# Kernel tuning notes

Measured on AMD Instinct MI355X. Metric: run time of the kernel, lower is better.

## Reference

```python
import jax, jax.numpy as jnp
import numpy as np

N_NODES = 20000
N_EDGES = 100000   # undirected input edges; make_directed doubles them
FEAT = 128
N_RBF = 20
NUM_CONV = 3
CUTOFF = 20.0
BOX = 10.0


def setup_inputs() -> dict:
    key = jax.random.key(0)
    ks = jax.random.split(key, 6)
    cg_xyz = jax.random.uniform(ks[0], (N_NODES, 3), jnp.float32) * BOX
    # random edges with no self-loops (avoid d=0 singularity in rbf/unit)
    src = jax.random.randint(ks[1], (N_EDGES,), 0, N_NODES)
    off = jax.random.randint(ks[2], (N_EDGES,), 1, N_NODES)
    CG_nbr_list = jnp.stack([src, (src + off) % N_NODES], axis=1)
    cg_s = jax.random.normal(ks[3], (N_NODES, FEAT), jnp.float32)

    def w(k, shape, fan_in):
        return (jax.random.normal(k, shape, jnp.float32) / np.float32(np.sqrt(fan_in)))
    kk = jax.random.split(ks[4], 7)
    params = dict(
        msg_W1=w(kk[0], (NUM_CONV, FEAT, FEAT), FEAT),
        msg_b1=jnp.zeros((NUM_CONV, FEAT), jnp.float32),
        msg_W2=w(kk[1], (NUM_CONV, 3 * FEAT, FEAT), FEAT),
        msg_b2=jnp.zeros((NUM_CONV, 3 * FEAT), jnp.float32),
        dist_W=w(kk[2], (NUM_CONV, 3 * FEAT, N_RBF), N_RBF),
        dist_b=jnp.zeros((NUM_CONV, 3 * FEAT), jnp.float32),
        upd_U=w(kk[3], (NUM_CONV, FEAT, FEAT), FEAT),
        upd_V=w(kk[4], (NUM_CONV, FEAT, FEAT), FEAT),
        upd_sW1=w(kk[5], (NUM_CONV, FEAT, 2 * FEAT), 2 * FEAT),
        upd_sb1=jnp.zeros((NUM_CONV, FEAT), jnp.float32),
        upd_sW2=w(kk[6], (NUM_CONV, 3 * FEAT, FEAT), FEAT),
        upd_sb2=jnp.zeros((NUM_CONV, 3 * FEAT), jnp.float32),
    )
    return dict(cg_xyz=cg_xyz, CG_nbr_list=CG_nbr_list, cg_s=cg_s, **params)


def _forward(cg_xyz, cg_s, nbr, msg_W1, msg_b1, msg_W2, msg_b2, dist_W, dist_b,
             upd_U, upd_V, upd_sW1, upd_sb1, upd_sW2, upd_sb2):
    N = cg_s.shape[0]
    # make_directed: input is undirected -> append flipped edges
    nbrs = jnp.concatenate([nbr, nbr[:, ::-1]], axis=0)   # [E, 2]
    i, j = nbrs[:, 0], nbrs[:, 1]
    r_ij = cg_xyz[j] - cg_xyz[i]                           # [E, 3]
    d = jnp.linalg.norm(r_ij, axis=-1)                     # [E]
    unit = r_ij / d[:, None]
    # PainnRadialBasis: sin(k*pi*d/cutoff)/d, k=1..n_rbf
    kvec = jnp.arange(1, N_RBF + 1, dtype=cg_xyz.dtype)
    rbf = jnp.sin(kvec * jnp.pi * d[:, None] / CUTOFF) / d[:, None]   # [E, n_rbf]
    # cosine envelope
    env = jnp.where(d < CUTOFF, 0.5 * (jnp.cos(jnp.pi * d / CUTOFF) + 1.0), 0.0)

    s = cg_s
    v = jnp.zeros((N, FEAT, 3), cg_s.dtype)
    for l in range(NUM_CONV):
        # ---- MessageBlock ----
        phi = jax.nn.silu(s @ msg_W1[l].T + msg_b1[l]) @ msg_W2[l].T + msg_b2[l]  # [N, 3F]
        w_s = (rbf @ dist_W[l].T + dist_b[l]) * env[:, None]                      # [E, 3F]
        inv = (phi[j] * w_s).reshape(-1, 3, FEAT)                                 # [E, 3, F]
        dv_ij = inv[:, 2, :, None] * unit[:, None, :] + inv[:, 0, :, None] * v[j] # [E, F, 3]
        s = s + jax.ops.segment_sum(inv[:, 1, :], i, num_segments=N)
        v = v + jax.ops.segment_sum(dv_ij, i, num_segments=N)
        # ---- UpdateBlock ----
        u_v = jnp.einsum('nfd,gf->ngd', v, upd_U[l])   # [N, F, 3]
        v_v = jnp.einsum('nfd,gf->ngd', v, upd_V[l])
        v_v_norm = jnp.linalg.norm(v_v, axis=-1)       # [N, F]
        a = (jax.nn.silu(jnp.concatenate([s, v_v_norm], -1) @ upd_sW1[l].T + upd_sb1[l])
             @ upd_sW2[l].T + upd_sb2[l]).reshape(-1, 3, FEAT)  # a_vv, a_sv, a_ss
        s = s + (u_v * v_v).sum(-1) * a[:, 1, :] + a[:, 2, :]
        v = v + u_v * a[:, 0, :, None]
    return s, v


def reference(cg_xyz, CG_nbr_list, cg_s, msg_W1, msg_b1, msg_W2, msg_b2, dist_W,
              dist_b, upd_U, upd_V, upd_sW1, upd_sb1, upd_sW2, upd_sb2):
    return _forward(cg_xyz, cg_s, CG_nbr_list, msg_W1, msg_b1, msg_W2, msg_b2,
                    dist_W, dist_b, upd_U, upd_V, upd_sW1, upd_sb1, upd_sW2, upd_sb2)
```

## Files before the change

### kernel.cpp

```cpp
#include <hip/hip_runtime.h>
#include <math.h>

#define FEAT 128
#define NRBF 20
#define NCONV 3
#define PI_F 3.14159265358979323846f

typedef __attribute__((ext_vector_type(8))) short short8;
typedef __attribute__((ext_vector_type(4))) float floatx4;
typedef unsigned short ushort_t;

__device__ inline float b2f(unsigned short u) {
    union { unsigned int i; float f; } c; c.i = ((unsigned int)u) << 16; return c.f;
}
__device__ inline unsigned short f2b(float x) {
    union { float f; unsigned int i; } c; c.f = x;
    unsigned int u = c.i;
    return (unsigned short)((u + 0x7fffu + ((u >> 16) & 1u)) >> 16);
}

template<int MODE>
__global__ __launch_bounds__(256, 2) void mlp_fused_kernel(
    const float* __restrict__ s, const float* __restrict__ vv,
    const ushort_t* __restrict__ W1h, const ushort_t* __restrict__ W1l,
    const float* __restrict__ b1,
    const ushort_t* __restrict__ W2h, const ushort_t* __restrict__ W2l,
    const float* __restrict__ b2,
    ushort_t* __restrict__ out_b,
    const float* __restrict__ uv,
    float* s_out, float* vbuf,
    float* outv,
    const ushort_t* __restrict__ pW1h, const ushort_t* __restrict__ pW1l,
    const float* __restrict__ pb1,
    const ushort_t* __restrict__ pW2h, const ushort_t* __restrict__ pW2l,
    const float* __restrict__ pb2,
    ushort_t* __restrict__ pout,
    int M, int K1, int SP)
{
    __shared__ __align__(16) ushort_t Ah[64 * 40];
    __shared__ __align__(16) ushort_t Al[64 * 40];
    __shared__ __align__(16) ushort_t Wh[128 * 40];
    __shared__ __align__(16) ushort_t Wl[128 * 40];
    __shared__ __align__(16) ushort_t Hh[64 * 136];
    __shared__ __align__(16) ushort_t Hl[64 * 136];

    const int t    = threadIdx.x;
    const int m0   = blockIdx.x * 64;
    const int wv   = t >> 6;
    const int lane = t & 63;
    const int wn   = wv * 32;
    const int lr   = lane & 15;
    const int lk   = (lane >> 4) * 8;
    const int quad = lane >> 4;
    const int arow = t >> 3;
    const int acol = (t & 7) * 4;
    const int wrow = t >> 2;
    const int wcol = (t & 3) * 8;

    floatx4 acc[4][2] = {};

    for (int k0 = 0; k0 < K1; k0 += 32) {
        #pragma unroll
        for (int h = 0; h < 2; ++h) {
            int r = arow + h * 32;
            int m = m0 + r; if (m >= M) m = M - 1;
            float xs[4];
            if (k0 < 128) {
                float4 av = *(const float4*)(s + (long)m * 128 + k0 + acol);
                xs[0] = av.x; xs[1] = av.y; xs[2] = av.z; xs[3] = av.w;
            } else {
                long base = (long)m * 128 + (k0 - 128 + acol);
                float4 a0 = *(const float4*)(vv + base);
                float4 a1 = *(const float4*)(vv + (long)SP + base);
                float4 a2 = *(const float4*)(vv + 2 * (long)SP + base);
                xs[0] = sqrtf(a0.x * a0.x + a1.x * a1.x + a2.x * a2.x);
                xs[1] = sqrtf(a0.y * a0.y + a1.y * a1.y + a2.y * a2.y);
                xs[2] = sqrtf(a0.z * a0.z + a1.z * a1.z + a2.z * a2.z);
                xs[3] = sqrtf(a0.w * a0.w + a1.w * a1.w + a2.w * a2.w);
            }
            unsigned short hh[4], ll[4];
            #pragma unroll
            for (int q = 0; q < 4; ++q) {
                hh[q] = f2b(xs[q]);
                ll[q] = f2b(xs[q] - b2f(hh[q]));
            }
            *(ushort4*)(&Ah[r * 40 + acol]) = make_ushort4(hh[0], hh[1], hh[2], hh[3]);
            *(ushort4*)(&Al[r * 40 + acol]) = make_ushort4(ll[0], ll[1], ll[2], ll[3]);
        }
        #pragma unroll
        for (int h = 0; h < 2; ++h) {
            int r = wrow + h * 64;
            *(uint4*)(&Wh[r * 40 + wcol]) =
                *(const uint4*)(W1h + (long)r * K1 + k0 + wcol);
            *(uint4*)(&Wl[r * 40 + wcol]) =
                *(const uint4*)(W1l + (long)r * K1 + k0 + wcol);
        }
        __syncthreads();
        short8 af[4], alf[4], wf[2], wlf[2];
        #pragma unroll
        for (int i = 0; i < 4; ++i) {
            af[i]  = *(const short8*)(&Ah[(i * 16 + lr) * 40 + lk]);
            alf[i] = *(const short8*)(&Al[(i * 16 + lr) * 40 + lk]);
        }
        #pragma unroll
        for (int j = 0; j < 2; ++j) {
            wf[j]  = *(const short8*)(&Wh[(wn + j * 16 + lr) * 40 + lk]);
            wlf[j] = *(const short8*)(&Wl[(wn + j * 16 + lr) * 40 + lk]);
        }
        #pragma unroll
        for (int i = 0; i < 4; ++i)
            #pragma unroll
            for (int j = 0; j < 2; ++j) {
                acc[i][j] = __builtin_amdgcn_mfma_f32_16x16x32_bf16(
                    af[i], wf[j], acc[i][j], 0, 0, 0);
                acc[i][j] = __builtin_amdgcn_mfma_f32_16x16x32_bf16(
                    af[i], wlf[j], acc[i][j], 0, 0, 0);
                acc[i][j] = __builtin_amdgcn_mfma_f32_16x16x32_bf16(
                    alf[i], wf[j], acc[i][j], 0, 0, 0);
            }
        __syncthreads();
    }

    #pragma unroll
    for (int i = 0; i < 4; ++i)
        #pragma unroll
        for (int r = 0; r < 4; ++r) {
            int mrow = i * 16 + quad * 4 + r;
            #pragma unroll
            for (int j = 0; j < 2; ++j) {
                int kcol = wn + j * 16 + lr;
                float x = acc[i][j][r] + b1[kcol];
                x *= 1.f / (1.f + __expf(-x));
                unsigned short hh = f2b(x);
                Hh[mrow * 136 + kcol] = hh;
                Hl[mrow * 136 + kcol] = f2b(x - b2f(hh));
            }
        }

    floatx4 accS[3][4][2];
    #pragma unroll
    for (int nt = 0; nt < 3; ++nt) {
        floatx4 a2c[4][2] = {};
        for (int k0 = 0; k0 < 128; k0 += 32) {
            __syncthreads();
            #pragma unroll
            for (int h = 0; h < 2; ++h) {
                int r = wrow + h * 64;
                long wo = (long)(nt * 128 + r) * 128;
                *(uint4*)(&Wh[r * 40 + wcol]) = *(const uint4*)(W2h + wo + k0 + wcol);
                *(uint4*)(&Wl[r * 40 + wcol]) = *(const uint4*)(W2l + wo + k0 + wcol);
            }
            __syncthreads();
            short8 af[4], alf[4], wf[2], wlf[2];
            #pragma unroll
            for (int i = 0; i < 4; ++i) {
                af[i]  = *(const short8*)(&Hh[(i * 16 + lr) * 136 + k0 + lk]);
                alf[i] = *(const short8*)(&Hl[(i * 16 + lr) * 136 + k0 + lk]);
            }
            #pragma unroll
            for (int j = 0; j < 2; ++j) {
                wf[j]  = *(const short8*)(&Wh[(wn + j * 16 + lr) * 40 + lk]);
                wlf[j] = *(const short8*)(&Wl[(wn + j * 16 + lr) * 40 + lk]);
            }
            #pragma unroll
            for (int i = 0; i < 4; ++i)
                #pragma unroll
                for (int j = 0; j < 2; ++j) {
                    a2c[i][j] = __builtin_amdgcn_mfma_f32_16x16x32_bf16(
                        af[i], wf[j], a2c[i][j], 0, 0, 0);
                    a2c[i][j] = __builtin_amdgcn_mfma_f32_16x16x32_bf16(
                        af[i], wlf[j], a2c[i][j], 0, 0, 0);
                    a2c[i][j] = __builtin_amdgcn_mfma_f32_16x16x32_bf16(
                        alf[i], wf[j], a2c[i][j], 0, 0, 0);
                }
        }
        if (MODE >= 1) {
            #pragma unroll
            for (int i = 0; i < 4; ++i)
                #pragma unroll
                for (int j = 0; j < 2; ++j)
                    accS[nt][i][j] = a2c[i][j];
        } else {
            #pragma unroll
            for (int i = 0; i < 4; ++i)
                #pragma unroll
                for (int r = 0; r < 4; ++r) {
                    int m = m0 + i * 16 + quad * 4 + r;
                    if (m >= M) continue;
                    #pragma unroll
                    for (int j = 0; j < 2; ++j) {
                        int n = nt * 128 + wn + j * 16 + lr;
                        out_b[(long)m * 384 + n] = f2b(a2c[i][j][r] + b2[n]);
                    }
                }
        }
    }

    if (MODE >= 1) {
        if (MODE == 2) __syncthreads();
        #pragma unroll
        for (int i = 0; i < 4; ++i)
            #pragma unroll
            for (int r = 0; r < 4; ++r) {
                int m = m0 + i * 16 + quad * 4 + r;
                if (m >= M) continue;
                #pragma unroll
                for (int j = 0; j < 2; ++j) {
                    int g = wn + j * 16 + lr;
                    long idx = (long)m * 128 + g;
                    float a0 = accS[0][i][j][r] + b2[g];
                    float a1 = accS[1][i][j][r] + b2[128 + g];
                    float a2 = accS[2][i][j][r] + b2[256 + g];
                    float u0 = uv[idx], u1 = uv[SP + idx], u2 = uv[2 * SP + idx];
                    float w0 = vv[idx], w1 = vv[SP + idx], w2 = vv[2 * SP + idx];
                    float dot = u0 * w0 + u1 * w1 + u2 * w2;
                    float sn = s[idx] + dot * a1 + a2;
                    s_out[idx] = sn;
                    if (MODE == 2) {
                        int mrow = i * 16 + quad * 4 + r;
                        unsigned short sh = f2b(sn);
                        Hh[mrow * 136 + g] = sh;
                        Hl[mrow * 136 + g] = f2b(sn - b2f(sh));
                    }
                    float x0 = vbuf[idx]          + u0 * a0;
                    float x1 = vbuf[SP + idx]     + u1 * a0;
                    float x2 = vbuf[2 * SP + idx] + u2 * a0;
                    if (MODE == 1 && outv) {
                        outv[idx * 3 + 0] = x0;
                        outv[idx * 3 + 1] = x1;
                        outv[idx * 3 + 2] = x2;
                    } else {
                        vbuf[idx]          = x0;
                        vbuf[SP + idx]     = x1;
                        vbuf[2 * SP + idx] = x2;
                    }
                }
            }
    }

    if (MODE == 2) {
        __syncthreads();
        floatx4 pacc[4][2] = {};
        for (int k0 = 0; k0 < 128; k0 += 32) {
            __syncthreads();
            #pragma unroll
            for (int h = 0; h < 2; ++h) {
                int r = wrow + h * 64;
                *(uint4*)(&Wh[r * 40 + wcol]) =
                    *(const uint4*)(pW1h + (long)r * 128 + k0 + wcol);
                *(uint4*)(&Wl[r * 40 + wcol]) =
                    *(const uint4*)(pW1l + (long)r * 128 + k0 + wcol);
            }
            __syncthreads();
            short8 af[4], alf[4], wf[2], wlf[2];
            #pragma unroll
            for (int i = 0; i < 4; ++i) {
                af[i]  = *(const short8*)(&Hh[(i * 16 + lr) * 136 + k0 + lk]);
                alf[i] = *(const short8*)(&Hl[(i * 16 + lr) * 136 + k0 + lk]);
            }
            #pragma unroll
            for (int j = 0; j < 2; ++j) {
                wf[j]  = *(const short8*)(&Wh[(wn + j * 16 + lr) * 40 + lk]);
                wlf[j] = *(const short8*)(&Wl[(wn + j * 16 + lr) * 40 + lk]);
            }
            #pragma unroll
            for (int i = 0; i < 4; ++i)
                #pragma unroll
                for (int j = 0; j < 2; ++j) {
                    pacc[i][j] = __builtin_amdgcn_mfma_f32_16x16x32_bf16(
                        af[i], wf[j], pacc[i][j], 0, 0, 0);
                    pacc[i][j] = __builtin_amdgcn_mfma_f32_16x16x32_bf16(
                        af[i], wlf[j], pacc[i][j], 0, 0, 0);
                    pacc[i][j] = __builtin_amdgcn_mfma_f32_16x16x32_bf16(
                        alf[i], wf[j], pacc[i][j], 0, 0, 0);
                }
        }
        __syncthreads();
        #pragma unroll
        for (int i = 0; i < 4; ++i)
            #pragma unroll
            for (int r = 0; r < 4; ++r) {
                int mrow = i * 16 + quad * 4 + r;
                #pragma unroll
                for (int j = 0; j < 2; ++j) {
                    int kcol = wn + j * 16 + lr;
                    float x = pacc[i][j][r] + pb1[kcol];
                    x *= 1.f / (1.f + __expf(-x));
                    unsigned short hh = f2b(x);
                    Hh[mrow * 136 + kcol] = hh;
                    Hl[mrow * 136 + kcol] = f2b(x - b2f(hh));
                }
            }
        for (int nt = 0; nt < 3; ++nt) {
            floatx4 c2[4][2] = {};
            for (int k0 = 0; k0 < 128; k0 += 32) {
                __syncthreads();
                #pragma unroll
                for (int h = 0; h < 2; ++h) {
                    int r = wrow + h * 64;
                    long wo = (long)(nt * 128 + r) * 128;
                    *(uint4*)(&Wh[r * 40 + wcol]) =
                        *(const uint4*)(pW2h + wo + k0 + wcol);
                    *(uint4*)(&Wl[r * 40 + wcol]) =
                        *(const uint4*)(pW2l + wo + k0 + wcol);
                }
                __syncthreads();
                short8 af[4], alf[4], wf[2], wlf[2];
                #pragma unroll
                for (int i = 0; i < 4; ++i) {
                    af[i]  = *(const short8*)(&Hh[(i * 16 + lr) * 136 + k0 + lk]);
                    alf[i] = *(const short8*)(&Hl[(i * 16 + lr) * 136 + k0 + lk]);
                }
                #pragma unroll
                for (int j = 0; j < 2; ++j) {
                    wf[j]  = *(const short8*)(&Wh[(wn + j * 16 + lr) * 40 + lk]);
                    wlf[j] = *(const short8*)(&Wl[(wn + j * 16 + lr) * 40 + lk]);
                }
                #pragma unroll
                for (int i = 0; i < 4; ++i)
                    #pragma unroll
                    for (int j = 0; j < 2; ++j) {
                        c2[i][j] = __builtin_amdgcn_mfma_f32_16x16x32_bf16(
                            af[i], wf[j], c2[i][j], 0, 0, 0);
                        c2[i][j] = __builtin_amdgcn_mfma_f32_16x16x32_bf16(
                            af[i], wlf[j], c2[i][j], 0, 0, 0);
                        c2[i][j] = __builtin_amdgcn_mfma_f32_16x16x32_bf16(
                            alf[i], wf[j], c2[i][j], 0, 0, 0);
                    }
            }
            #pragma unroll
            for (int i = 0; i < 4; ++i)
                #pragma unroll
                for (int r = 0; r < 4; ++r) {
                    int m = m0 + i * 16 + quad * 4 + r;
                    if (m >= M) continue;
                    #pragma unroll
                    for (int j = 0; j < 2; ++j) {
                        int n = nt * 128 + wn + j * 16 + lr;
                        pout[(long)m * 384 + n] = f2b(c2[i][j][r] + pb2[n]);
                    }
                }
        }
    }
}

__global__ __launch_bounds__(256) void gemm_ps_kernel(
    const ushort_t* __restrict__ Ahg, const ushort_t* __restrict__ Alg,
    const ushort_t* __restrict__ Whi, const ushort_t* __restrict__ Wlo,
    const ushort_t* __restrict__ W2h, const ushort_t* __restrict__ W2l,
    float* __restrict__ C0, float* __restrict__ C1,
    int M, int K)
{
    __shared__ __align__(16) ushort_t Ah[128 * 40];
    __shared__ __align__(16) ushort_t Al[128 * 40];
    __shared__ __align__(16) ushort_t Wh[128 * 40];
    __shared__ __align__(16) ushort_t Wl[128 * 40];
    const int t    = threadIdx.x;
    const int m0   = blockIdx.x * 128;
    const int nt   = blockIdx.y;
    const int wv   = t >> 6;
    const int lane = t & 63;
    const int wm   = (wv >> 1) * 64;
    const int wn   = (wv & 1) * 64;
    const int lr   = lane & 15;
    const int lk   = (lane >> 4) * 8;
    const int srow = t >> 2;
    const int scol = (t & 3) * 8;
    const ushort_t* Wsh = nt ? W2h : Whi;
    const ushort_t* Wsl = nt ? W2l : Wlo;

    floatx4 acc[4][4] = {};

    for (int k0 = 0; k0 < K; k0 += 32) {
        #pragma unroll
        for (int h = 0; h < 2; ++h) {
            int r = srow + h * 64;
            int m = m0 + r; if (m >= M) m = M - 1;
            *(uint4*)(&Ah[r * 40 + scol]) =
                *(const uint4*)(Ahg + (long)m * K + k0 + scol);
            *(uint4*)(&Al[r * 40 + scol]) =
                *(const uint4*)(Alg + (long)m * K + k0 + scol);
            *(uint4*)(&Wh[r * 40 + scol]) =
                *(const uint4*)(Wsh + (long)r * K + k0 + scol);
            *(uint4*)(&Wl[r * 40 + scol]) =
                *(const uint4*)(Wsl + (long)r * K + k0 + scol);
        }
        __syncthreads();
        short8 ah[4], al[4], wh[4], wl[4];
        #pragma unroll
        for (int i = 0; i < 4; ++i) {
            ah[i] = *(const short8*)(&Ah[(wm + i * 16 + lr) * 40 + lk]);
            al[i] = *(const short8*)(&Al[(wm + i * 16 + lr) * 40 + lk]);
            wh[i] = *(const short8*)(&Wh[(wn + i * 16 + lr) * 40 + lk]);
            wl[i] = *(const short8*)(&Wl[(wn + i * 16 + lr) * 40 + lk]);
        }
        #pragma unroll
        for (int i = 0; i < 4; ++i)
            #pragma unroll
            for (int j = 0; j < 4; ++j) {
                acc[i][j] = __builtin_amdgcn_mfma_f32_16x16x32_bf16(
                    ah[i], wh[j], acc[i][j], 0, 0, 0);
                acc[i][j] = __builtin_amdgcn_mfma_f32_16x16x32_bf16(
                    ah[i], wl[j], acc[i][j], 0, 0, 0);
                acc[i][j] = __builtin_amdgcn_mfma_f32_16x16x32_bf16(
                    al[i], wh[j], acc[i][j], 0, 0, 0);
            }
        __syncthreads();
    }

    float* C = nt ? C1 : C0;
    #pragma unroll
    for (int i = 0; i < 4; ++i)
        #pragma unroll
        for (int r = 0; r < 4; ++r) {
            int m = m0 + wm + i * 16 + (lane >> 4) * 4 + r;
            if (m >= M) continue;
            #pragma unroll
            for (int j = 0; j < 4; ++j) {
                int n = wn + j * 16 + lr;
                C[(long)m * 128 + n] = acc[i][j][r];
            }
        }
}

__global__ __launch_bounds__(256) void split_kernel(
    const float* __restrict__ src, ushort_t* __restrict__ hi,
    ushort_t* __restrict__ lo, int n)
{
    int i = blockIdx.x * blockDim.x + threadIdx.x;
    if (i >= n) return;
    float x = src[i];
    unsigned short h = f2b(x);
    hi[i] = h;
    lo[i] = f2b(x - b2f(h));
}

__global__ __launch_bounds__(256) void hist_kernel(
    const int* __restrict__ nbr, int* __restrict__ deg, int Ed)
{
    int e = blockIdx.x * blockDim.x + threadIdx.x;
    if (e >= Ed) return;
    int E = Ed >> 1;
    int i = (e < E) ? nbr[2 * e] : nbr[2 * (e - E) + 1];
    atomicAdd(&deg[i], 1);
}

__device__ inline int wave_incl_scan(int x, int lane)
{
    #pragma unroll
    for (int s = 1; s < 64; s <<= 1) {
        int y = __shfl_up(x, s, 64);
        if (lane >= s) x += y;
    }
    return x;
}

__global__ __launch_bounds__(1024) void scan_kernel(
    const int* __restrict__ deg, int* __restrict__ off,
    int* __restrict__ cursor, int N)
{
    __shared__ int wsum[16];
    __shared__ int carry_s;
    const int t = threadIdx.x;
    const int lane = t & 63;
    const int w = t >> 6;
    if (t == 0) { carry_s = 0; off[0] = 0; }
    __syncthreads();
    for (int base = 0; base < N; base += 1024) {
        int i = base + t;
        int x = (i < N) ? deg[i] : 0;
        int sc = wave_incl_scan(x, lane);
        if (lane == 63) wsum[w] = sc;
        __syncthreads();
        if (w == 0) {
            int v = (lane < 16) ? wsum[lane] : 0;
            int vs = wave_incl_scan(v, lane);
            if (lane < 16) wsum[lane] = vs;
        }
        __syncthreads();
        int waveoff = (w > 0) ? wsum[w - 1] : 0;
        int inc = sc + waveoff + carry_s;
        if (i < N) { off[i + 1] = inc; cursor[i] = inc - x; }
        __syncthreads();
        if (t == 1023) carry_s = inc;
        __syncthreads();
    }
}

__global__ __launch_bounds__(256) void scatter_geom_kernel(
    const int* __restrict__ nbr, const float* __restrict__ xyz,
    int* __restrict__ cursor, int* __restrict__ csr_j,
    float* __restrict__ csr_env, float* __restrict__ csr_unit,
    float* __restrict__ csr_rbfe, int Ed)
{
    int e = blockIdx.x * blockDim.x + threadIdx.x;
    if (e >= Ed) return;
    int E = Ed >> 1;
    int i, j;
    if (e < E) { i = nbr[2 * e];         j = nbr[2 * e + 1]; }
    else       { int u = e - E; i = nbr[2 * u + 1]; j = nbr[2 * u]; }

    int p = atomicAdd(&cursor[i], 1);
    csr_j[p] = j;

    float rx = xyz[3 * j + 0] - xyz[3 * i + 0];
    float ry = xyz[3 * j + 1] - xyz[3 * i + 1];
    float rz = xyz[3 * j + 2] - xyz[3 * i + 2];
    float d   = sqrtf(rx * rx + ry * ry + rz * rz);
    float inv = 1.f / d;
    csr_unit[3 * p + 0] = rx * inv;
    csr_unit[3 * p + 1] = ry * inv;
    csr_unit[3 * p + 2] = rz * inv;
    float ev = (d < 20.f) ? 0.5f * (__cosf(PI_F * d / 20.f) + 1.f) : 0.f;
    csr_env[p] = ev;
    float base = PI_F * d / 20.f;
    #pragma unroll
    for (int k = 0; k < NRBF; ++k)
        csr_rbfe[(long)p * NRBF + k] = ev * __sinf((float)(k + 1) * base) * inv;
}

__global__ __launch_bounds__(128) void edge_aggr_kernel(
    const int* __restrict__ off, const int* __restrict__ csr_j,
    const float* __restrict__ csr_env, const float* __restrict__ csr_unit,
    const float* __restrict__ csr_rbfe,
    const ushort_t* __restrict__ phib, const float* __restrict__ vold,
    const float* __restrict__ distW, const float* __restrict__ distb,
    float* __restrict__ s, float* __restrict__ vnew,
    ushort_t* __restrict__ vnh, ushort_t* __restrict__ vnl, int N, int SP)
{
    const int f = threadIdx.x;
    float w0c[NRBF], w1c[NRBF], w2c[NRBF];
    const float b0 = distb[f];
    const float b1 = distb[128 + f];
    const float b2 = distb[256 + f];
    #pragma unroll
    for (int k = 0; k < NRBF; ++k) {
        w0c[k] = distW[(long)f * NRBF + k];
        w1c[k] = distW[(long)(128 + f) * NRBF + k];
        w2c[k] = distW[(long)(256 + f) * NRBF + k];
    }

    for (int node = blockIdx.x; node < N; node += gridDim.x) {
        const int p0 = off[node], p1 = off[node + 1];
        float ssum = 0.f, v0 = 0.f, v1 = 0.f, v2 = 0.f;
        for (int p = p0; p < p1; ++p) {
            int j = csr_j[p];
            float ev = csr_env[p];
            float ux = csr_unit[3 * p + 0];
            float uy = csr_unit[3 * p + 1];
            float uz = csr_unit[3 * p + 2];
            const float* rb = csr_rbfe + (long)p * NRBF;
            float w0 = ev * b0, w1 = ev * b1, w2 = ev * b2;
            #pragma unroll
            for (int k = 0; k < NRBF; ++k) {
                float r = rb[k];
                w0 += r * w0c[k];
                w1 += r * w1c[k];
                w2 += r * w2c[k];
            }
            long jb = (long)j * 384;
            float i0 = b2f(phib[jb + f])       * w0;
            float i1 = b2f(phib[jb + 128 + f]) * w1;
            float i2 = b2f(phib[jb + 256 + f]) * w2;
            long jv = (long)j * FEAT + f;
            ssum += i1;
            v0 += i2 * ux + i0 * vold[jv];
            v1 += i2 * uy + i0 * vold[SP + jv];
            v2 += i2 * uz + i0 * vold[2 * SP + jv];
        }
        long iv = (long)node * FEAT + f;
        s[iv] += ssum;
        float n0 = vold[iv]          + v0;
        float n1 = vold[SP + iv]     + v1;
        float n2 = vold[2 * SP + iv] + v2;
        vnew[iv]          = n0;
        vnew[SP + iv]     = n1;
        vnew[2 * SP + iv] = n2;
        unsigned short h0 = f2b(n0), h1 = f2b(n1), h2 = f2b(n2);
        vnh[iv]          = h0;  vnl[iv]          = f2b(n0 - b2f(h0));
        vnh[SP + iv]     = h1;  vnl[SP + iv]     = f2b(n1 - b2f(h1));
        vnh[2 * SP + iv] = h2;  vnl[2 * SP + iv] = f2b(n2 - b2f(h2));
    }
}

__global__ __launch_bounds__(256) void init_s_kernel(
    const float* __restrict__ cg_s, float* __restrict__ s,
    float* __restrict__ vA, int nS, int nV)
{
    int idx = blockIdx.x * blockDim.x + threadIdx.x;
    if (idx < nS) s[idx] = cg_s[idx];
    if (idx < nV) vA[idx] = 0.f;
}

extern "C" void kernel_launch(void* const* d_in, const int* in_sizes, int n_in,
                              void* d_out, int out_size, void* d_ws, size_t ws_size,
                              hipStream_t stream)
{
    const float* xyz     = (const float*)d_in[0];
    const int*   nbr     = (const int*)  d_in[1];
    const float* cg_s    = (const float*)d_in[2];
    const float* msg_W1  = (const float*)d_in[3];
    const float* msg_b1  = (const float*)d_in[4];
    const float* msg_W2  = (const float*)d_in[5];
    const float* msg_b2  = (const float*)d_in[6];
    const float* dist_W  = (const float*)d_in[7];
    const float* dist_b  = (const float*)d_in[8];
    const float* upd_U   = (const float*)d_in[9];
    const float* upd_V   = (const float*)d_in[10];
    const float* upd_sW1 = (const float*)d_in[11];
    const float* upd_sb1 = (const float*)d_in[12];
    const float* upd_sW2 = (const float*)d_in[13];
    const float* upd_sb2 = (const float*)d_in[14];

    const int E  = in_sizes[1] / 2;
    const int Ed = 2 * E;
    const int N  = in_sizes[2] / FEAT;
    const int SP = N * FEAT;

    float* s    = (float*)d_out;
    float* outv = (float*)d_out + (long)SP;

    float* w = (float*)d_ws;
    size_t off_ = 0;
    auto alloc = [&](size_t nelem) {
        float* p = w + off_;
        off_ += (nelem + 255) & ~(size_t)255;
        return p;
    };
    auto allocb = [&](size_t nelem) {
        return (ushort_t*)alloc((nelem + 1) / 2);
    };
    int*   deg      = (int*)alloc((size_t)N);
    int*   off      = (int*)alloc((size_t)N + 1);
    int*   cursor   = (int*)alloc((size_t)N);
    int*   csr_j    = (int*)alloc((size_t)Ed);
    float* csr_env  = alloc((size_t)Ed);
    float* csr_unit = alloc((size_t)Ed * 3);
    float* csr_rbfe = alloc((size_t)Ed * NRBF);
    float* u_v      = alloc((size_t)3 * SP);
    float* v_v      = alloc((size_t)3 * SP);
    float* vA       = alloc((size_t)3 * SP);
    float* vB       = alloc((size_t)3 * SP);
    ushort_t* phi_b = allocb((size_t)N * 384);
    ushort_t* vnh   = allocb((size_t)3 * SP);
    ushort_t* vnl   = allocb((size_t)3 * SP);
    const int n1 = NCONV * FEAT * FEAT;
    const int n2 = NCONV * 3 * FEAT * FEAT;
    const int n3 = NCONV * FEAT * 2 * FEAT;
    ushort_t* w1h  = allocb((size_t)n1);
    ushort_t* w1l  = allocb((size_t)n1);
    ushort_t* w2h  = allocb((size_t)n2);
    ushort_t* w2l  = allocb((size_t)n2);
    ushort_t* uh   = allocb((size_t)n1);
    ushort_t* ul   = allocb((size_t)n1);
    ushort_t* vh   = allocb((size_t)n1);
    ushort_t* vl   = allocb((size_t)n1);
    ushort_t* sw1h = allocb((size_t)n3);
    ushort_t* sw1l = allocb((size_t)n3);
    ushort_t* sw2h = allocb((size_t)n2);
    ushort_t* sw2l = allocb((size_t)n2);
    (void)ws_size; (void)n_in; (void)out_size;

    split_kernel<<<(n1 + 255) / 256, 256, 0, stream>>>(msg_W1, w1h, w1l, n1);
    split_kernel<<<(n2 + 255) / 256, 256, 0, stream>>>(msg_W2, w2h, w2l, n2);
    split_kernel<<<(n1 + 255) / 256, 256, 0, stream>>>(upd_U, uh, ul, n1);
    split_kernel<<<(n1 + 255) / 256, 256, 0, stream>>>(upd_V, vh, vl, n1);
    split_kernel<<<(n3 + 255) / 256, 256, 0, stream>>>(upd_sW1, sw1h, sw1l, n3);
    split_kernel<<<(n2 + 255) / 256, 256, 0, stream>>>(upd_sW2, sw2h, sw2l, n2);

    {
        int n = 3 * SP;
        init_s_kernel<<<(n + 255) / 256, 256, 0, stream>>>(cg_s, s, vA, SP, n);
    }

    hipMemsetAsync(deg, 0, (size_t)N * sizeof(int), stream);
    hist_kernel<<<(Ed + 255) / 256, 256, 0, stream>>>(nbr, deg, Ed);
    scan_kernel<<<1, 1024, 0, stream>>>(deg, off, cursor, N);
    scatter_geom_kernel<<<(Ed + 255) / 256, 256, 0, stream>>>(
        nbr, xyz, cursor, csr_j, csr_env, csr_unit, csr_rbfe, Ed);

    float* vold = vA;
    float* vnew = vB;
    dim3 gM((N + 63) / 64, 1);
    dim3 gUV((3 * N + 127) / 128, 2);
    int edgeGrid = 2048;
    if (edgeGrid > N) edgeGrid = N;

    for (int l = 0; l < NCONV; ++l) {
        const float* b2  = msg_b2  + (long)l * 3 * FEAT;
        const float* dW  = dist_W  + (long)l * 3 * FEAT * NRBF;
        const float* db  = dist_b  + (long)l * 3 * FEAT;
        const float* sb1 = upd_sb1 + (long)l * FEAT;
        const float* sb2 = upd_sb2 + (long)l * 3 * FEAT;
        const long o1 = (long)l * FEAT * FEAT;
        const long o2 = (long)l * 3 * FEAT * FEAT;
        const long o3 = (long)l * FEAT * 2 * FEAT;

        if (l == 0) {
            const float* b1 = msg_b1;
            mlp_fused_kernel<0><<<gM, 256, 0, stream>>>(
                s, nullptr, w1h, w1l, b1, w2h, w2l, b2,
                phi_b, nullptr, nullptr, nullptr, nullptr,
                nullptr, nullptr, nullptr, nullptr, nullptr, nullptr, nullptr,
                N, FEAT, SP);
        }

        edge_aggr_kernel<<<edgeGrid, 128, 0, stream>>>(
            off, csr_j, csr_env, csr_unit, csr_rbfe, phi_b, vold,
            dW, db, s, vnew, vnh, vnl, N, SP);

        gemm_ps_kernel<<<gUV, 256, 0, stream>>>(
            vnh, vnl, uh + o1, ul + o1, vh + o1, vl + o1,
            u_v, v_v, 3 * N, FEAT);

        if (l < NCONV - 1) {
            const long o1n = (long)(l + 1) * FEAT * FEAT;
            const long o2n = (long)(l + 1) * 3 * FEAT * FEAT;
            const float* pb1 = msg_b1 + (long)(l + 1) * FEAT;
            const float* pb2 = msg_b2 + (long)(l + 1) * 3 * FEAT;
            mlp_fused_kernel<2><<<gM, 256, 0, stream>>>(
                s, v_v, sw1h + o3, sw1l + o3, sb1, sw2h + o2, sw2l + o2, sb2,
                nullptr, u_v, s, vnew, nullptr,
                w1h + o1n, w1l + o1n, pb1, w2h + o2n, w2l + o2n, pb2, phi_b,
                N, 2 * FEAT, SP);
        } else {
            mlp_fused_kernel<1><<<gM, 256, 0, stream>>>(
                s, v_v, sw1h + o3, sw1l + o3, sb1, sw2h + o2, sw2l + o2, sb2,
                nullptr, u_v, s, vnew, outv,
                nullptr, nullptr, nullptr, nullptr, nullptr, nullptr, nullptr,
                N, 2 * FEAT, SP);
        }

        float* tmp = vold; vold = vnew; vnew = tmp;
    }
}
```

Measured before the change: 760.4 us.

## Interleave vector components per node and fuse U/V GEMM with dot and norm epilogue

The edge kernel now writes the bf16 hi/lo split of v as four padded rows per node (x,y,z,zero). A single GEMM computes both U·v and V·v over these rows, so each thread's MFMA accumulator holds the three components of one node/feature. That lets the epilogue compute u·v and |V v| directly and write a float4 (u,dot) plus a norm array. The MLP kernel then reads these precomputed values instead of gathering six strided component arrays and recomputing the norms. The cost is a third more GEMM rows spent on padding, double the weight tiles in shared memory, and extra memsets of the padded buffers.

```diff
diff --git a/kernel.cpp b/kernel.cpp
--- a/kernel.cpp
+++ b/kernel.cpp
@@ -21,13 +21,13 @@
 
 template<int MODE>
 __global__ __launch_bounds__(256, 2) void mlp_fused_kernel(
-    const float* __restrict__ s, const float* __restrict__ vv,
+    const float* __restrict__ s, const float* __restrict__ nrm,
     const ushort_t* __restrict__ W1h, const ushort_t* __restrict__ W1l,
     const float* __restrict__ b1,
     const ushort_t* __restrict__ W2h, const ushort_t* __restrict__ W2l,
     const float* __restrict__ b2,
     ushort_t* __restrict__ out_b,
-    const float* __restrict__ uv,
+    const float4* __restrict__ uvd,
     float* s_out, float* vbuf,
     float* outv,
     const ushort_t* __restrict__ pW1h, const ushort_t* __restrict__ pW1l,
@@ -69,14 +69,8 @@
                 float4 av = *(const float4*)(s + (long)m * 128 + k0 + acol);
                 xs[0] = av.x; xs[1] = av.y; xs[2] = av.z; xs[3] = av.w;
             } else {
-                long base = (long)m * 128 + (k0 - 128 + acol);
-                float4 a0 = *(const float4*)(vv + base);
-                float4 a1 = *(const float4*)(vv + (long)SP + base);
-                float4 a2 = *(const float4*)(vv + 2 * (long)SP + base);
-                xs[0] = sqrtf(a0.x * a0.x + a1.x * a1.x + a2.x * a2.x);
-                xs[1] = sqrtf(a0.y * a0.y + a1.y * a1.y + a2.y * a2.y);
-                xs[2] = sqrtf(a0.z * a0.z + a1.z * a1.z + a2.z * a2.z);
-                xs[3] = sqrtf(a0.w * a0.w + a1.w * a1.w + a2.w * a2.w);
+                float4 av = *(const float4*)(nrm + (long)m * 128 + (k0 - 128) + acol);
+                xs[0] = av.x; xs[1] = av.y; xs[2] = av.z; xs[3] = av.w;
             }
             unsigned short hh[4], ll[4];
             #pragma unroll
@@ -211,10 +205,8 @@
                     float a0 = accS[0][i][j][r] + b2[g];
                     float a1 = accS[1][i][j][r] + b2[128 + g];
                     float a2 = accS[2][i][j][r] + b2[256 + g];
-                    float u0 = uv[idx], u1 = uv[SP + idx], u2 = uv[2 * SP + idx];
-                    float w0 = vv[idx], w1 = vv[SP + idx], w2 = vv[2 * SP + idx];
-                    float dot = u0 * w0 + u1 * w1 + u2 * w2;
-                    float sn = s[idx] + dot * a1 + a2;
+                    float4 ud = uvd[idx];
+                    float sn = s[idx] + ud.w * a1 + a2;
                     s_out[idx] = sn;
                     if (MODE == 2) {
                         int mrow = i * 16 + quad * 4 + r;
@@ -222,9 +214,9 @@
                         Hh[mrow * 136 + g] = sh;
                         Hl[mrow * 136 + g] = f2b(sn - b2f(sh));
                     }
-                    float x0 = vbuf[idx]          + u0 * a0;
-                    float x1 = vbuf[SP + idx]     + u1 * a0;
-                    float x2 = vbuf[2 * SP + idx] + u2 * a0;
+                    float x0 = vbuf[idx]          + ud.x * a0;
+                    float x1 = vbuf[SP + idx]     + ud.y * a0;
+                    float x2 = vbuf[2 * SP + idx] + ud.z * a0;
                     if (MODE == 1 && outv) {
                         outv[idx * 3 + 0] = x0;
                         outv[idx * 3 + 1] = x1;
@@ -344,83 +336,93 @@
     }
 }
 
-__global__ __launch_bounds__(256) void gemm_ps_kernel(
+__global__ __launch_bounds__(256, 2) void gemm_uv_kernel(
     const ushort_t* __restrict__ Ahg, const ushort_t* __restrict__ Alg,
-    const ushort_t* __restrict__ Whi, const ushort_t* __restrict__ Wlo,
-    const ushort_t* __restrict__ W2h, const ushort_t* __restrict__ W2l,
-    float* __restrict__ C0, float* __restrict__ C1,
-    int M, int K)
+    const ushort_t* __restrict__ Uh, const ushort_t* __restrict__ Ul,
+    const ushort_t* __restrict__ Vh, const ushort_t* __restrict__ Vl,
+    float4* __restrict__ uvd, float* __restrict__ nrm,
+    int Mr)
 {
     __shared__ __align__(16) ushort_t Ah[128 * 40];
     __shared__ __align__(16) ushort_t Al[128 * 40];
-    __shared__ __align__(16) ushort_t Wh[128 * 40];
-    __shared__ __align__(16) ushort_t Wl[128 * 40];
+    __shared__ __align__(16) ushort_t WUh[128 * 40];
+    __shared__ __align__(16) ushort_t WUl[128 * 40];
+    __shared__ __align__(16) ushort_t WVh[128 * 40];
+    __shared__ __align__(16) ushort_t WVl[128 * 40];
     const int t    = threadIdx.x;
     const int m0   = blockIdx.x * 128;
-    const int nt   = blockIdx.y;
     const int wv   = t >> 6;
     const int lane = t & 63;
     const int wm   = (wv >> 1) * 64;
     const int wn   = (wv & 1) * 64;
     const int lr   = lane & 15;
     const int lk   = (lane >> 4) * 8;
+    const int quad = lane >> 4;
     const int srow = t >> 2;
     const int scol = (t & 3) * 8;
-    const ushort_t* Wsh = nt ? W2h : Whi;
-    const ushort_t* Wsl = nt ? W2l : Wlo;
-
-    floatx4 acc[4][4] = {};
-
-    for (int k0 = 0; k0 < K; k0 += 32) {
+
+    floatx4 aU[4][4] = {};
+    floatx4 aV[4][4] = {};
+
+    for (int k0 = 0; k0 < 128; k0 += 32) {
         #pragma unroll
         for (int h = 0; h < 2; ++h) {
             int r = srow + h * 64;
-            int m = m0 + r; if (m >= M) m = M - 1;
-            *(uint4*)(&Ah[r * 40 + scol]) =
-                *(const uint4*)(Ahg + (long)m * K + k0 + scol);
-            *(uint4*)(&Al[r * 40 + scol]) =
-                *(const uint4*)(Alg + (long)m * K + k0 + scol);
-            *(uint4*)(&Wh[r * 40 + scol]) =
-                *(const uint4*)(Wsh + (long)r * K + k0 + scol);
-            *(uint4*)(&Wl[r * 40 + scol]) =
-                *(const uint4*)(Wsl + (long)r * K + k0 + scol);
-        }
-        __syncthreads();
-        short8 ah[4], al[4], wh[4], wl[4];
+            int m = m0 + r; if (m >= Mr) m = Mr - 1;
+            *(uint4*)(&Ah[r * 40 + scol])  = *(const uint4*)(Ahg + (long)m * 128 + k0 + scol);
+            *(uint4*)(&Al[r * 40 + scol])  = *(const uint4*)(Alg + (long)m * 128 + k0 + scol);
+            *(uint4*)(&WUh[r * 40 + scol]) = *(const uint4*)(Uh + (long)r * 128 + k0 + scol);
+            *(uint4*)(&WUl[r * 40 + scol]) = *(const uint4*)(Ul + (long)r * 128 + k0 + scol);
+            *(uint4*)(&WVh[r * 40 + scol]) = *(const uint4*)(Vh + (long)r * 128 + k0 + scol);
+            *(uint4*)(&WVl[r * 40 + scol]) = *(const uint4*)(Vl + (long)r * 128 + k0 + scol);
+        }
+        __syncthreads();
+        short8 ah[4], al[4];
         #pragma unroll
         for (int i = 0; i < 4; ++i) {
             ah[i] = *(const short8*)(&Ah[(wm + i * 16 + lr) * 40 + lk]);
             al[i] = *(const short8*)(&Al[(wm + i * 16 + lr) * 40 + lk]);
-            wh[i] = *(const short8*)(&Wh[(wn + i * 16 + lr) * 40 + lk]);
-            wl[i] = *(const short8*)(&Wl[(wn + i * 16 + lr) * 40 + lk]);
-        }
-        #pragma unroll
-        for (int i = 0; i < 4; ++i)
-            #pragma unroll
-            for (int j = 0; j < 4; ++j) {
-                acc[i][j] = __builtin_amdgcn_mfma_f32_16x16x32_bf16(
-                    ah[i], wh[j], acc[i][j], 0, 0, 0);
-                acc[i][j] = __builtin_amdgcn_mfma_f32_16x16x32_bf16(
-                    ah[i], wl[j], acc[i][j], 0, 0, 0);
-                acc[i][j] = __builtin_amdgcn_mfma_f32_16x16x32_bf16(
-                    al[i], wh[j], acc[i][j], 0, 0, 0);
-            }
-        __syncthreads();
-    }
-
-    float* C = nt ? C1 : C0;
+        }
+        #pragma unroll
+        for (int j = 0; j < 4; ++j) {
+            short8 wuh = *(const short8*)(&WUh[(wn + j * 16 + lr) * 40 + lk]);
+            short8 wul = *(const short8*)(&WUl[(wn + j * 16 + lr) * 40 + lk]);
+            short8 wvh = *(const short8*)(&WVh[(wn + j * 16 + lr) * 40 + lk]);
+            short8 wvl = *(const short8*)(&WVl[(wn + j * 16 + lr) * 40 + lk]);
+            #pragma unroll
+            for (int i = 0; i < 4; ++i) {
+                aU[i][j] = __builtin_amdgcn_mfma_f32_16x16x32_bf16(
+                    ah[i], wuh, aU[i][j], 0, 0, 0);
+                aU[i][j] = __builtin_amdgcn_mfma_f32_16x16x32_bf16(
+                    ah[i], wul, aU[i][j], 0, 0, 0);
+                aU[i][j] = __builtin_amdgcn_mfma_f32_16x16x32_bf16(
+                    al[i], wuh, aU[i][j], 0, 0, 0);
+                aV[i][j] = __builtin_amdgcn_mfma_f32_16x16x32_bf16(
+                    ah[i], wvh, aV[i][j], 0, 0, 0);
+                aV[i][j] = __builtin_amdgcn_mfma_f32_16x16x32_bf16(
+                    ah[i], wvl, aV[i][j], 0, 0, 0);
+                aV[i][j] = __builtin_amdgcn_mfma_f32_16x16x32_bf16(
+                    al[i], wvh, aV[i][j], 0, 0, 0);
+            }
+        }
+        __syncthreads();
+    }
+
     #pragma unroll
-    for (int i = 0; i < 4; ++i)
-        #pragma unroll
-        for (int r = 0; r < 4; ++r) {
-            int m = m0 + wm + i * 16 + (lane >> 4) * 4 + r;
-            if (m >= M) continue;
-            #pragma unroll
-            for (int j = 0; j < 4; ++j) {
-                int n = wn + j * 16 + lr;
-                C[(long)m * 128 + n] = acc[i][j][r];
-            }
-        }
+    for (int i = 0; i < 4; ++i) {
+        int mbase = m0 + wm + i * 16 + quad * 4;
+        if (mbase >= Mr) continue;
+        int node = mbase >> 2;
+        #pragma unroll
+        for (int j = 0; j < 4; ++j) {
+            int n = wn + j * 16 + lr;
+            float u0 = aU[i][j][0], u1 = aU[i][j][1], u2 = aU[i][j][2];
+            float w0 = aV[i][j][0], w1 = aV[i][j][1], w2 = aV[i][j][2];
+            float dot = u0 * w0 + u1 * w1 + u2 * w2;
+            uvd[(long)node * 128 + n] = make_float4(u0, u1, u2, dot);
+            nrm[(long)node * 128 + n] = sqrtf(w0 * w0 + w1 * w1 + w2 * w2);
+        }
+    }
 }
 
 __global__ __launch_bounds__(256) void split_kernel(
@@ -577,9 +579,10 @@
         vnew[SP + iv]     = n1;
         vnew[2 * SP + iv] = n2;
         unsigned short h0 = f2b(n0), h1 = f2b(n1), h2 = f2b(n2);
-        vnh[iv]          = h0;  vnl[iv]          = f2b(n0 - b2f(h0));
-        vnh[SP + iv]     = h1;  vnl[SP + iv]     = f2b(n1 - b2f(h1));
-        vnh[2 * SP + iv] = h2;  vnl[2 * SP + iv] = f2b(n2 - b2f(h2));
+        long ib = (long)node * 512 + f;
+        vnh[ib]       = h0;  vnl[ib]       = f2b(n0 - b2f(h0));
+        vnh[ib + 128] = h1;  vnl[ib + 128] = f2b(n1 - b2f(h1));
+        vnh[ib + 256] = h2;  vnl[ib + 256] = f2b(n2 - b2f(h2));
     }
 }
 
@@ -637,13 +640,13 @@
     float* csr_env  = alloc((size_t)Ed);
     float* csr_unit = alloc((size_t)Ed * 3);
     float* csr_rbfe = alloc((size_t)Ed * NRBF);
-    float* u_v      = alloc((size_t)3 * SP);
-    float* v_v      = alloc((size_t)3 * SP);
+    float* uvd      = alloc((size_t)4 * SP);
+    float* nrm      = alloc((size_t)SP);
     float* vA       = alloc((size_t)3 * SP);
     float* vB       = alloc((size_t)3 * SP);
     ushort_t* phi_b = allocb((size_t)N * 384);
-    ushort_t* vnh   = allocb((size_t)3 * SP);
-    ushort_t* vnl   = allocb((size_t)3 * SP);
+    ushort_t* vnh   = allocb((size_t)4 * SP);
+    ushort_t* vnl   = allocb((size_t)4 * SP);
     const int n1 = NCONV * FEAT * FEAT;
     const int n2 = NCONV * 3 * FEAT * FEAT;
     const int n3 = NCONV * FEAT * 2 * FEAT;
@@ -671,6 +674,8 @@
     {
         int n = 3 * SP;
         init_s_kernel<<<(n + 255) / 256, 256, 0, stream>>>(cg_s, s, vA, SP, n);
+        hipMemsetAsync(vnh, 0, (size_t)4 * SP * sizeof(ushort_t), stream);
+        hipMemsetAsync(vnl, 0, (size_t)4 * SP * sizeof(ushort_t), stream);
     }
 
     hipMemsetAsync(deg, 0, (size_t)N * sizeof(int), stream);
@@ -682,7 +687,7 @@
     float* vold = vA;
     float* vnew = vB;
     dim3 gM((N + 63) / 64, 1);
-    dim3 gUV((3 * N + 127) / 128, 2);
+    dim3 gUV((4 * N + 127) / 128, 1);
     int edgeGrid = 2048;
     if (edgeGrid > N) edgeGrid = N;
 
@@ -709,9 +714,9 @@
             off, csr_j, csr_env, csr_unit, csr_rbfe, phi_b, vold,
             dW, db, s, vnew, vnh, vnl, N, SP);
 
-        gemm_ps_kernel<<<gUV, 256, 0, stream>>>(
+        gemm_uv_kernel<<<gUV, 256, 0, stream>>>(
             vnh, vnl, uh + o1, ul + o1, vh + o1, vl + o1,
-            u_v, v_v, 3 * N, FEAT);
+            (float4*)uvd, nrm, 4 * N);
 
         if (l < NCONV - 1) {
             const long o1n = (long)(l + 1) * FEAT * FEAT;
@@ -719,14 +724,14 @@
             const float* pb1 = msg_b1 + (long)(l + 1) * FEAT;
             const float* pb2 = msg_b2 + (long)(l + 1) * 3 * FEAT;
             mlp_fused_kernel<2><<<gM, 256, 0, stream>>>(
-                s, v_v, sw1h + o3, sw1l + o3, sb1, sw2h + o2, sw2l + o2, sb2,
-                nullptr, u_v, s, vnew, nullptr,
+                s, nrm, sw1h + o3, sw1l + o3, sb1, sw2h + o2, sw2l + o2, sb2,
+                nullptr, (const float4*)uvd, s, vnew, nullptr,
                 w1h + o1n, w1l + o1n, pb1, w2h + o2n, w2l + o2n, pb2, phi_b,
                 N, 2 * FEAT, SP);
         } else {
             mlp_fused_kernel<1><<<gM, 256, 0, stream>>>(
-                s, v_v, sw1h + o3, sw1l + o3, sb1, sw2h + o2, sw2l + o2, sb2,
-                nullptr, u_v, s, vnew, outv,
+                s, nrm, sw1h + o3, sw1l + o3, sb1, sw2h + o2, sw2l + o2, sb2,
+                nullptr, (const float4*)uvd, s, vnew, outv,
                 nullptr, nullptr, nullptr, nullptr, nullptr, nullptr, nullptr,
                 N, 2 * FEAT, SP);
         }
```

Result: no change. 751.8 us (median of 3 runs) (-1.1%).
